# Kernel tuning notes

Measured on AMD Instinct MI355X. Metric: run time of the kernel, lower is better.

Reference implementation:

```python
import jax, jax.numpy as jnp
import numpy as np

EPS = 1e-5  # BatchNorm eps (eval mode, uses running stats)


def _conv1x1(x, W, b):
    # x: [B,C,H,W], W: [O,C], b: [O] -> [B,O,H,W]
    return jnp.einsum('bchw,oc->bohw', x, W) + b[None, :, None, None]


def setup_inputs() -> dict:
    key = jax.random.key(0)
    ks = jax.random.split(key, 13)
    B, C, M, N = 16, 512, 64, 64
    CR = C // 2
    s = 0.02
    return {
        'x': jax.random.normal(ks[0], (B, C, M, N), dtype=jnp.float32),
        'Wq': jax.random.normal(ks[1], (CR, C), dtype=jnp.float32) * s,
        'bq': jax.random.normal(ks[2], (CR,), dtype=jnp.float32) * s,
        'Wk': jax.random.normal(ks[3], (CR, C), dtype=jnp.float32) * s,
        'bk': jax.random.normal(ks[4], (CR,), dtype=jnp.float32) * s,
        'Wv': jax.random.normal(ks[5], (CR, C), dtype=jnp.float32) * s,
        'bv': jax.random.normal(ks[6], (CR,), dtype=jnp.float32) * s,
        'Wr': jax.random.normal(ks[7], (C, CR), dtype=jnp.float32) * s,
        'br': jax.random.normal(ks[8], (C,), dtype=jnp.float32) * s,
        'gamma': jax.random.normal(ks[9], (C,), dtype=jnp.float32) * 0.1 + 1.0,
        'beta': jax.random.normal(ks[10], (C,), dtype=jnp.float32) * 0.1,
        'running_mean': jax.random.normal(ks[11], (C,), dtype=jnp.float32) * 0.1,
        'running_var': jax.random.uniform(ks[12], (C,), dtype=jnp.float32, minval=0.5, maxval=1.5),
    }


def reference(x, Wq, bq, Wk, bk, Wv, bv, Wr, br, gamma, beta, running_mean, running_var):
    b, c, m, n = x.shape
    cr = Wq.shape[0]
    # 1x1-conv QKV projections
    Q = _conv1x1(x, Wq, bq).reshape(b * cr, m, n)
    K = _conv1x1(x, Wk, bk).reshape(b * cr, m, n)
    V = _conv1x1(x, Wv, bv).reshape(b * cr, m, n)
    # per-channel spatial attention over rows: [b*cr, m, m]
    corr = jnp.einsum('gik,gjk->gij', Q, K)
    attn = jax.nn.softmax(corr, axis=-1)
    y = jnp.einsum('gij,gjn->gin', attn, V).reshape(b, cr, m, n)
    # reconstruct: 1x1 conv + BatchNorm (eval mode) + residual
    y = _conv1x1(y, Wr, br)
    inv = gamma / jnp.sqrt(running_var + EPS)
    y = y * inv[None, :, None, None] + (beta - running_mean * inv)[None, :, None, None]
    return y + x
```

## Files before the change

kernel.cpp:

```cpp
#include <hip/hip_runtime.h>

typedef __attribute__((ext_vector_type(8))) short bf16x8;
typedef __attribute__((ext_vector_type(4))) float f32x4;

#define DEVI static __device__ __forceinline__

DEVI unsigned short f2b(float f) {
  union { float f; unsigned u; } v; v.f = f;
  unsigned r = v.u + 0x7fffu + ((v.u >> 16) & 1u);
  return (unsigned short)(r >> 16);
}

typedef const __attribute__((address_space(1))) void* gas1_t;
typedef __attribute__((address_space(3))) void* las3_t;
#define GL16(g, l) __builtin_amdgcn_global_load_lds((gas1_t)(g), (las3_t)(l), 16, 0, 0)

#define WAITVM(N) asm volatile("s_waitcnt vmcnt(" #N ")" ::: "memory")
#define WAITLGKM  asm volatile("s_waitcnt lgkmcnt(0)" ::: "memory")

#define OFF_WQKV  0ull
#define OFF_WR    786432ull
#define OFF_BQKV  1048576ull
#define OFF_SCALE 1051648ull
#define OFF_OFF2  1053696ull
#define OFF_XT    2097152ull
#define OFF_YT    2097152ull
#define OFF_Y     35651584ull
#define OFF_Q     69206016ull

__global__ __launch_bounds__(256) void k_prep(
    const float* __restrict__ Wq, const float* __restrict__ bq,
    const float* __restrict__ Wk, const float* __restrict__ bk,
    const float* __restrict__ Wv, const float* __restrict__ bv,
    const float* __restrict__ Wr, const float* __restrict__ br,
    const float* __restrict__ gamma, const float* __restrict__ beta,
    const float* __restrict__ rm, const float* __restrict__ rv,
    unsigned short* __restrict__ wqkv, unsigned short* __restrict__ wrb,
    float* __restrict__ bqkv, float* __restrict__ scale, float* __restrict__ off2)
{
  int i = blockIdx.x * 256 + threadIdx.x;
  if (i < 768 * 512) {
    int o = i >> 9, c = i & 511;
    float v = (o < 256) ? Wq[o * 512 + c] : (o < 512 ? Wk[(o - 256) * 512 + c] : Wv[(o - 512) * 512 + c]);
    wqkv[i] = f2b(v);
  }
  if (i < 512 * 256) wrb[i] = f2b(Wr[i]);
  if (i < 768) bqkv[i] = (i < 256) ? bq[i] : (i < 512 ? bk[i - 256] : bv[i - 512]);
  if (i < 512) {
    float inv = gamma[i] * rsqrtf(rv[i] + 1e-5f);
    scale[i] = inv;
    off2[i] = (br[i] - rm[i]) * inv + beta[i];
  }
}

__global__ __launch_bounds__(256) void k_xt(const float* __restrict__ x, unsigned short* __restrict__ xt)
{
  __shared__ unsigned short tile[64][72];
  const int b = blockIdx.z, c0 = blockIdx.y * 64, s0 = blockIdx.x * 64;
  const int t = threadIdx.x;
  const int r = t >> 2, cc = (t & 3) * 16;
  const float* src = x + ((size_t)b * 512 + c0 + r) * 4096 + s0 + cc;
  #pragma unroll
  for (int j = 0; j < 16; j += 4) {
    float4 v = *(const float4*)(src + j);
    tile[r][cc + j + 0] = f2b(v.x);
    tile[r][cc + j + 1] = f2b(v.y);
    tile[r][cc + j + 2] = f2b(v.z);
    tile[r][cc + j + 3] = f2b(v.w);
  }
  __syncthreads();
  unsigned short* dst = xt + ((size_t)b * 4096 + s0 + r) * 512 + c0 + cc;
  bf16x8 o0, o1;
  #pragma unroll
  for (int j = 0; j < 8; ++j) { o0[j] = tile[cc + j][r]; o1[j] = tile[cc + 8 + j][r]; }
  *(bf16x8*)(dst) = o0;
  *(bf16x8*)(dst + 8) = o1;
}


__global__ __launch_bounds__(256) void k_qkv(
    const unsigned short* __restrict__ xt, const unsigned short* __restrict__ wqkv,
    const float* __restrict__ bqkv, unsigned short* __restrict__ qkv)
{
  __shared__ unsigned short lds[2][2][8192];
  const int b = blockIdx.z, o0 = blockIdx.y * 128, s0 = blockIdx.x * 128;
  const int t = threadIdx.x, w = t >> 6, l = t & 63;
  const int wm = w >> 1, wn = w & 1, lr = l & 15;
  const int lkE = (l >> 4) * 8;
  const int swE = (lr & 7) * 8;
  const int cp = (t & 7) ^ ((t >> 3) & 7);

  const unsigned short* Ag = wqkv + (size_t)(o0 + (t >> 3)) * 512 + cp * 8;
  const unsigned short* Bg = xt + ((size_t)b * 4096 + s0 + (t >> 3)) * 512 + cp * 8;

  const f32x4 z = {0.f, 0.f, 0.f, 0.f};
  f32x4 acc[4][4];
  #pragma unroll
  for (int i = 0; i < 4; ++i)
    #pragma unroll
    for (int j = 0; j < 4; ++j) acc[i][j] = z;

#define STG_Q(st, kt) do { \
    _Pragma("unroll") \
    for (int j = 0; j < 4; ++j) { \
      GL16(Ag + (kt) * 64 + j * 32 * 512, (char*)&lds[st][0][0] + j * 4096 + t * 16); \
      GL16(Bg + (kt) * 64 + j * 32 * 512, (char*)&lds[st][1][0] + j * 4096 + t * 16); \
    } \
  } while (0)

#define CMP_Q(st) do { \
    const unsigned short* A  = &lds[st][0][0]; \
    const unsigned short* Bl = &lds[st][1][0]; \
    _Pragma("unroll") \
    for (int kc = 0; kc < 2; ++kc) { \
      const int kidx = (kc * 32 + lkE) ^ swE; \
      bf16x8 af[4], bfr[4]; \
      _Pragma("unroll") \
      for (int mi = 0; mi < 4; ++mi) af[mi] = *(const bf16x8*)(A + (wm * 64 + mi * 16 + lr) * 64 + kidx); \
      _Pragma("unroll") \
      for (int ni = 0; ni < 4; ++ni) bfr[ni] = *(const bf16x8*)(Bl + (wn * 64 + ni * 16 + lr) * 64 + kidx); \
      _Pragma("unroll") \
      for (int mi = 0; mi < 4; ++mi) \
        _Pragma("unroll") \
        for (int ni = 0; ni < 4; ++ni) \
          acc[mi][ni] = __builtin_amdgcn_mfma_f32_16x16x32_bf16(af[mi], bfr[ni], acc[mi][ni], 0, 0, 0); \
    } \
    WAITLGKM; __builtin_amdgcn_sched_barrier(0); \
  } while (0)

  STG_Q(0, 0); STG_Q(1, 1);
  #pragma unroll
  for (int kt = 0; kt < 7; ++kt) {
    WAITVM(8);
    __builtin_amdgcn_s_barrier();
    CMP_Q(kt & 1);
    if (kt + 2 < 8) {
      __builtin_amdgcn_s_barrier();
      STG_Q(kt & 1, kt + 2);
    }
  }
  WAITVM(0);
  __builtin_amdgcn_s_barrier();
  CMP_Q(1);

  #pragma unroll
  for (int mi = 0; mi < 4; ++mi) {
    #pragma unroll
    for (int reg = 0; reg < 4; ++reg) {
      const int o = o0 + wm * 64 + mi * 16 + (l >> 4) * 4 + reg;
      const float bias = bqkv[o];
      const size_t base = (size_t)(o >> 8) * 16777216ull + ((size_t)b * 256 + (o & 255)) * 4096;
      #pragma unroll
      for (int ni = 0; ni < 4; ++ni) {
        const int s = s0 + wn * 64 + ni * 16 + lr;
        qkv[base + s] = f2b(acc[mi][ni][reg] + bias);
      }
    }
  }
#undef STG_Q
#undef CMP_Q
}

__global__ __launch_bounds__(256) void k_attn(const unsigned short* __restrict__ qkv,
                                              unsigned short* __restrict__ yout)
{
  __shared__ unsigned short Vt[64][80];
  __shared__ unsigned short P[4][16][80];
  const int g = blockIdx.x;
  const unsigned short* qg = qkv + (size_t)g * 4096;
  const unsigned short* kg = qkv + 16777216ull + (size_t)g * 4096;
  const unsigned short* vg = qkv + 33554432ull + (size_t)g * 4096;
  const int t = threadIdx.x, w = t >> 6, l = t & 63;
  const int lr = l & 15, lk = (l >> 4) * 8;

  {
    const int j = t >> 2, c0 = (t & 3) * 16;
    bf16x8 a = *(const bf16x8*)(vg + j * 64 + c0);
    bf16x8 bb = *(const bf16x8*)(vg + j * 64 + c0 + 8);
    #pragma unroll
    for (int jj = 0; jj < 8; ++jj) { Vt[c0 + jj][j] = a[jj]; Vt[c0 + 8 + jj][j] = bb[jj]; }
  }

  const f32x4 z = {0.f, 0.f, 0.f, 0.f};
  bf16x8 qf[2];
  #pragma unroll
  for (int kc = 0; kc < 2; ++kc) qf[kc] = *(const bf16x8*)(qg + (w * 16 + lr) * 64 + kc * 32 + lk);
  f32x4 accS[4] = {z, z, z, z};
  #pragma unroll
  for (int jt = 0; jt < 4; ++jt)
    #pragma unroll
    for (int kc = 0; kc < 2; ++kc) {
      bf16x8 kf = *(const bf16x8*)(kg + (jt * 16 + lr) * 64 + kc * 32 + lk);
      accS[jt] = __builtin_amdgcn_mfma_f32_16x16x32_bf16(qf[kc], kf, accS[jt], 0, 0, 0);
    }

  #pragma unroll
  for (int reg = 0; reg < 4; ++reg) {
    float mx = fmaxf(fmaxf(accS[0][reg], accS[1][reg]), fmaxf(accS[2][reg], accS[3][reg]));
    #pragma unroll
    for (int m = 1; m < 16; m <<= 1) mx = fmaxf(mx, __shfl_xor(mx, m, 64));
    float e0 = __expf(accS[0][reg] - mx), e1 = __expf(accS[1][reg] - mx);
    float e2 = __expf(accS[2][reg] - mx), e3 = __expf(accS[3][reg] - mx);
    float sm = e0 + e1 + e2 + e3;
    #pragma unroll
    for (int m = 1; m < 16; m <<= 1) sm += __shfl_xor(sm, m, 64);
    const float rs = 1.f / sm;
    const int row = (l >> 4) * 4 + reg;
    P[w][row][0 * 16 + lr] = f2b(e0 * rs);
    P[w][row][1 * 16 + lr] = f2b(e1 * rs);
    P[w][row][2 * 16 + lr] = f2b(e2 * rs);
    P[w][row][3 * 16 + lr] = f2b(e3 * rs);
  }
  __syncthreads();

  bf16x8 pf[2];
  #pragma unroll
  for (int kc = 0; kc < 2; ++kc) pf[kc] = *(const bf16x8*)(&P[w][lr][kc * 32 + lk]);
  f32x4 accY[4] = {z, z, z, z};
  #pragma unroll
  for (int nt = 0; nt < 4; ++nt)
    #pragma unroll
    for (int kc = 0; kc < 2; ++kc) {
      bf16x8 vf = *(const bf16x8*)(&Vt[nt * 16 + lr][kc * 32 + lk]);
      accY[nt] = __builtin_amdgcn_mfma_f32_16x16x32_bf16(pf[kc], vf, accY[nt], 0, 0, 0);
    }

  unsigned short* yg = yout + (size_t)g * 4096;
  #pragma unroll
  for (int nt = 0; nt < 4; ++nt)
    #pragma unroll
    for (int reg = 0; reg < 4; ++reg) {
      const int i = w * 16 + (l >> 4) * 4 + reg;
      yg[i * 64 + nt * 16 + lr] = f2b(accY[nt][reg]);
    }
}

__global__ __launch_bounds__(256) void k_yt(const unsigned short* __restrict__ y, unsigned short* __restrict__ yt)
{
  __shared__ unsigned short tile[64][72];
  const int b = blockIdx.z, cr0 = blockIdx.y * 64, s0 = blockIdx.x * 64;
  const int t = threadIdx.x, r = t >> 2, c0 = (t & 3) * 16;
  const unsigned short* src = y + ((size_t)b * 256 + cr0 + r) * 4096 + s0 + c0;
  bf16x8 a = *(const bf16x8*)(src);
  bf16x8 bb = *(const bf16x8*)(src + 8);
  #pragma unroll
  for (int j = 0; j < 8; ++j) { tile[r][c0 + j] = a[j]; tile[r][c0 + 8 + j] = bb[j]; }
  __syncthreads();
  unsigned short* dst = yt + ((size_t)b * 4096 + s0 + r) * 256 + cr0 + c0;
  bf16x8 o0, o1;
  #pragma unroll
  for (int j = 0; j < 8; ++j) { o0[j] = tile[c0 + j][r]; o1[j] = tile[c0 + 8 + j][r]; }
  *(bf16x8*)(dst) = o0;
  *(bf16x8*)(dst + 8) = o1;
}

__global__ __launch_bounds__(256) void k_recon(
    const unsigned short* __restrict__ yt, const unsigned short* __restrict__ wrb,
    const float* __restrict__ scale, const float* __restrict__ off2,
    const float* __restrict__ x, float* __restrict__ out)
{
  __shared__ unsigned short lds[2][2][8192];
  const int b = blockIdx.z, o0 = blockIdx.y * 128, s0 = blockIdx.x * 128;
  const int t = threadIdx.x, w = t >> 6, l = t & 63;
  const int wm = w >> 1, wn = w & 1, lr = l & 15;
  const int lkE = (l >> 4) * 8;
  const int swE = (lr & 7) * 8;
  const int cp = (t & 7) ^ ((t >> 3) & 7);

  const unsigned short* Ag = wrb + (size_t)(o0 + (t >> 3)) * 256 + cp * 8;
  const unsigned short* Bg = yt + ((size_t)b * 4096 + s0 + (t >> 3)) * 256 + cp * 8;

  const f32x4 z = {0.f, 0.f, 0.f, 0.f};
  f32x4 acc[4][4];
  #pragma unroll
  for (int i = 0; i < 4; ++i)
    #pragma unroll
    for (int j = 0; j < 4; ++j) acc[i][j] = z;

#define STG_R(st, kt) do { \
    _Pragma("unroll") \
    for (int j = 0; j < 4; ++j) { \
      GL16(Ag + (kt) * 64 + j * 32 * 256, (char*)&lds[st][0][0] + j * 4096 + t * 16); \
      GL16(Bg + (kt) * 64 + j * 32 * 256, (char*)&lds[st][1][0] + j * 4096 + t * 16); \
    } \
  } while (0)

#define CMP_R(st) do { \
    const unsigned short* A  = &lds[st][0][0]; \
    const unsigned short* Bl = &lds[st][1][0]; \
    _Pragma("unroll") \
    for (int kc = 0; kc < 2; ++kc) { \
      const int kidx = (kc * 32 + lkE) ^ swE; \
      bf16x8 af[4], bfr[4]; \
      _Pragma("unroll") \
      for (int mi = 0; mi < 4; ++mi) af[mi] = *(const bf16x8*)(A + (wm * 64 + mi * 16 + lr) * 64 + kidx); \
      _Pragma("unroll") \
      for (int ni = 0; ni < 4; ++ni) bfr[ni] = *(const bf16x8*)(Bl + (wn * 64 + ni * 16 + lr) * 64 + kidx); \
      _Pragma("unroll") \
      for (int mi = 0; mi < 4; ++mi) \
        _Pragma("unroll") \
        for (int ni = 0; ni < 4; ++ni) \
          acc[mi][ni] = __builtin_amdgcn_mfma_f32_16x16x32_bf16(af[mi], bfr[ni], acc[mi][ni], 0, 0, 0); \
    } \
    WAITLGKM; __builtin_amdgcn_sched_barrier(0); \
  } while (0)

  STG_R(0, 0); STG_R(1, 1);
  #pragma unroll
  for (int kt = 0; kt < 3; ++kt) {
    WAITVM(8);
    __builtin_amdgcn_s_barrier();
    CMP_R(kt & 1);
    if (kt + 2 < 4) {
      __builtin_amdgcn_s_barrier();
      STG_R(kt & 1, kt + 2);
    }
  }
  WAITVM(0);
  __builtin_amdgcn_s_barrier();
  CMP_R(1);

  #pragma unroll
  for (int mi = 0; mi < 4; ++mi) {
    #pragma unroll
    for (int reg = 0; reg < 4; ++reg) {
      const int o = o0 + wm * 64 + mi * 16 + (l >> 4) * 4 + reg;
      const float sc = scale[o], of = off2[o];
      const size_t base = ((size_t)b * 512 + o) * 4096;
      #pragma unroll
      for (int ni = 0; ni < 4; ++ni) {
        const int s = s0 + wn * 64 + ni * 16 + lr;
        const size_t idx = base + s;
        out[idx] = acc[mi][ni][reg] * sc + of + x[idx];
      }
    }
  }
#undef STG_R
#undef CMP_R
}

extern "C" void kernel_launch(void* const* d_in, const int* in_sizes, int n_in,
                              void* d_out, int out_size, void* d_ws, size_t ws_size,
                              hipStream_t stream)
{
  const float* x     = (const float*)d_in[0];
  const float* Wq    = (const float*)d_in[1];
  const float* bq    = (const float*)d_in[2];
  const float* Wk    = (const float*)d_in[3];
  const float* bk    = (const float*)d_in[4];
  const float* Wv    = (const float*)d_in[5];
  const float* bv    = (const float*)d_in[6];
  const float* Wr    = (const float*)d_in[7];
  const float* br    = (const float*)d_in[8];
  const float* gamma = (const float*)d_in[9];
  const float* beta  = (const float*)d_in[10];
  const float* rm    = (const float*)d_in[11];
  const float* rv    = (const float*)d_in[12];

  char* ws = (char*)d_ws;
  unsigned short* wqkv  = (unsigned short*)(ws + OFF_WQKV);
  unsigned short* wrb   = (unsigned short*)(ws + OFF_WR);
  float* bqkv  = (float*)(ws + OFF_BQKV);
  float* scale = (float*)(ws + OFF_SCALE);
  float* off2  = (float*)(ws + OFF_OFF2);
  unsigned short* xt  = (unsigned short*)(ws + OFF_XT);
  unsigned short* yt  = (unsigned short*)(ws + OFF_YT);
  unsigned short* yb  = (unsigned short*)(ws + OFF_Y);
  unsigned short* qkv = (unsigned short*)(ws + OFF_Q);
  float* out = (float*)d_out;

  hipLaunchKernelGGL(k_prep, dim3(1536), dim3(256), 0, stream,
                     Wq, bq, Wk, bk, Wv, bv, Wr, br, gamma, beta, rm, rv,
                     wqkv, wrb, bqkv, scale, off2);
  hipLaunchKernelGGL(k_xt, dim3(64, 8, 16), dim3(256), 0, stream, x, xt);
  hipLaunchKernelGGL(k_qkv, dim3(32, 6, 16), dim3(256), 0, stream, xt, wqkv, bqkv, qkv);
  hipLaunchKernelGGL(k_attn, dim3(4096), dim3(256), 0, stream, qkv, yb);
  hipLaunchKernelGGL(k_yt, dim3(64, 4, 16), dim3(256), 0, stream, yb, yt);
  hipLaunchKernelGGL(k_recon, dim3(32, 4, 16), dim3(256), 0, stream, yt, wrb, scale, off2, x, out);
}
```

Before: 212.5 us.

## Fuse weight prep into transpose, drop y transpose by loading channel-major tiles in recon

Weight conversion and BN folding are merged into the x-transpose kernel, so one launch does both. The separate y transpose kernel is removed: the reconstruction GEMM now reads y in its native channel-major layout through registers into a padded LDS tile and gathers B fragments with strided scalar LDS reads. The QKV GEMM loop preloads both k-chunks' fragments before issuing MFMAs and places sched barriers around the barriers. This removes a kernel launch and a full write and read of y, in exchange for slower element-wise LDS gathers and more register pressure in recon.

```diff
diff --git a/kernel.cpp b/kernel.cpp
--- a/kernel.cpp
+++ b/kernel.cpp
@@ -17,6 +17,7 @@
 
 #define WAITVM(N) asm volatile("s_waitcnt vmcnt(" #N ")" ::: "memory")
 #define WAITLGKM  asm volatile("s_waitcnt lgkmcnt(0)" ::: "memory")
+#define SCHEDBAR  __builtin_amdgcn_sched_barrier(0)
 
 #define OFF_WQKV  0ull
 #define OFF_WR    786432ull
@@ -24,11 +25,11 @@
 #define OFF_SCALE 1051648ull
 #define OFF_OFF2  1053696ull
 #define OFF_XT    2097152ull
-#define OFF_YT    2097152ull
 #define OFF_Y     35651584ull
 #define OFF_Q     69206016ull
 
-__global__ __launch_bounds__(256) void k_prep(
+__global__ __launch_bounds__(256) void k_xt(
+    const float* __restrict__ x, unsigned short* __restrict__ xt,
     const float* __restrict__ Wq, const float* __restrict__ bq,
     const float* __restrict__ Wk, const float* __restrict__ bk,
     const float* __restrict__ Wv, const float* __restrict__ bv,
@@ -38,26 +39,27 @@
     unsigned short* __restrict__ wqkv, unsigned short* __restrict__ wrb,
     float* __restrict__ bqkv, float* __restrict__ scale, float* __restrict__ off2)
 {
-  int i = blockIdx.x * 256 + threadIdx.x;
-  if (i < 768 * 512) {
-    int o = i >> 9, c = i & 511;
-    float v = (o < 256) ? Wq[o * 512 + c] : (o < 512 ? Wk[(o - 256) * 512 + c] : Wv[(o - 512) * 512 + c]);
-    wqkv[i] = f2b(v);
-  }
-  if (i < 512 * 256) wrb[i] = f2b(Wr[i]);
-  if (i < 768) bqkv[i] = (i < 256) ? bq[i] : (i < 512 ? bk[i - 256] : bv[i - 512]);
-  if (i < 512) {
-    float inv = gamma[i] * rsqrtf(rv[i] + 1e-5f);
-    scale[i] = inv;
-    off2[i] = (br[i] - rm[i]) * inv + beta[i];
-  }
-}
-
-__global__ __launch_bounds__(256) void k_xt(const float* __restrict__ x, unsigned short* __restrict__ xt)
-{
   __shared__ unsigned short tile[64][72];
+  const int t = threadIdx.x;
+  const int bid = blockIdx.x + blockIdx.y * 64 + blockIdx.z * 512;
+
+  if (bid < 1536) {
+    int i = bid * 256 + t;
+    if (i < 768 * 512) {
+      int o = i >> 9, c = i & 511;
+      float v = (o < 256) ? Wq[o * 512 + c] : (o < 512 ? Wk[(o - 256) * 512 + c] : Wv[(o - 512) * 512 + c]);
+      wqkv[i] = f2b(v);
+    }
+    if (i < 512 * 256) wrb[i] = f2b(Wr[i]);
+    if (i < 768) bqkv[i] = (i < 256) ? bq[i] : (i < 512 ? bk[i - 256] : bv[i - 512]);
+    if (i < 512) {
+      float inv = gamma[i] * rsqrtf(rv[i] + 1e-5f);
+      scale[i] = inv;
+      off2[i] = (br[i] - rm[i]) * inv + beta[i];
+    }
+  }
+
   const int b = blockIdx.z, c0 = blockIdx.y * 64, s0 = blockIdx.x * 64;
-  const int t = threadIdx.x;
   const int r = t >> 2, cc = (t & 3) * 16;
   const float* src = x + ((size_t)b * 512 + c0 + r) * 4096 + s0 + cc;
   #pragma unroll
@@ -76,7 +78,6 @@
   *(bf16x8*)(dst) = o0;
   *(bf16x8*)(dst + 8) = o1;
 }
-
 
 __global__ __launch_bounds__(256) void k_qkv(
     const unsigned short* __restrict__ xt, const unsigned short* __restrict__ wqkv,
@@ -111,36 +112,35 @@
 #define CMP_Q(st) do { \
     const unsigned short* A  = &lds[st][0][0]; \
     const unsigned short* Bl = &lds[st][1][0]; \
+    bf16x8 af[2][4], bfr[2][4]; \
     _Pragma("unroll") \
     for (int kc = 0; kc < 2; ++kc) { \
       const int kidx = (kc * 32 + lkE) ^ swE; \
-      bf16x8 af[4], bfr[4]; \
-      _Pragma("unroll") \
-      for (int mi = 0; mi < 4; ++mi) af[mi] = *(const bf16x8*)(A + (wm * 64 + mi * 16 + lr) * 64 + kidx); \
-      _Pragma("unroll") \
-      for (int ni = 0; ni < 4; ++ni) bfr[ni] = *(const bf16x8*)(Bl + (wn * 64 + ni * 16 + lr) * 64 + kidx); \
+      _Pragma("unroll") \
+      for (int mi = 0; mi < 4; ++mi) af[kc][mi] = *(const bf16x8*)(A + (wm * 64 + mi * 16 + lr) * 64 + kidx); \
+      _Pragma("unroll") \
+      for (int ni = 0; ni < 4; ++ni) bfr[kc][ni] = *(const bf16x8*)(Bl + (wn * 64 + ni * 16 + lr) * 64 + kidx); \
+    } \
+    _Pragma("unroll") \
+    for (int kc = 0; kc < 2; ++kc) \
       _Pragma("unroll") \
       for (int mi = 0; mi < 4; ++mi) \
         _Pragma("unroll") \
         for (int ni = 0; ni < 4; ++ni) \
-          acc[mi][ni] = __builtin_amdgcn_mfma_f32_16x16x32_bf16(af[mi], bfr[ni], acc[mi][ni], 0, 0, 0); \
-    } \
-    WAITLGKM; __builtin_amdgcn_sched_barrier(0); \
+          acc[mi][ni] = __builtin_amdgcn_mfma_f32_16x16x32_bf16(af[kc][mi], bfr[kc][ni], acc[mi][ni], 0, 0, 0); \
   } while (0)
 
   STG_Q(0, 0); STG_Q(1, 1);
   #pragma unroll
   for (int kt = 0; kt < 7; ++kt) {
     WAITVM(8);
-    __builtin_amdgcn_s_barrier();
+    __builtin_amdgcn_s_barrier(); SCHEDBAR;
     CMP_Q(kt & 1);
-    if (kt + 2 < 8) {
-      __builtin_amdgcn_s_barrier();
-      STG_Q(kt & 1, kt + 2);
-    }
+    __builtin_amdgcn_s_barrier(); SCHEDBAR;
+    if (kt + 2 < 8) STG_Q(kt & 1, kt + 2);
   }
   WAITVM(0);
-  __builtin_amdgcn_s_barrier();
+  __builtin_amdgcn_s_barrier(); SCHEDBAR;
   CMP_Q(1);
 
   #pragma unroll
@@ -235,31 +235,13 @@
     }
 }
 
-__global__ __launch_bounds__(256) void k_yt(const unsigned short* __restrict__ y, unsigned short* __restrict__ yt)
-{
-  __shared__ unsigned short tile[64][72];
-  const int b = blockIdx.z, cr0 = blockIdx.y * 64, s0 = blockIdx.x * 64;
-  const int t = threadIdx.x, r = t >> 2, c0 = (t & 3) * 16;
-  const unsigned short* src = y + ((size_t)b * 256 + cr0 + r) * 4096 + s0 + c0;
-  bf16x8 a = *(const bf16x8*)(src);
-  bf16x8 bb = *(const bf16x8*)(src + 8);
-  #pragma unroll
-  for (int j = 0; j < 8; ++j) { tile[r][c0 + j] = a[j]; tile[r][c0 + 8 + j] = bb[j]; }
-  __syncthreads();
-  unsigned short* dst = yt + ((size_t)b * 4096 + s0 + r) * 256 + cr0 + c0;
-  bf16x8 o0, o1;
-  #pragma unroll
-  for (int j = 0; j < 8; ++j) { o0[j] = tile[c0 + j][r]; o1[j] = tile[c0 + 8 + j][r]; }
-  *(bf16x8*)(dst) = o0;
-  *(bf16x8*)(dst + 8) = o1;
-}
-
 __global__ __launch_bounds__(256) void k_recon(
-    const unsigned short* __restrict__ yt, const unsigned short* __restrict__ wrb,
+    const unsigned short* __restrict__ y, const unsigned short* __restrict__ wrb,
     const float* __restrict__ scale, const float* __restrict__ off2,
     const float* __restrict__ x, float* __restrict__ out)
 {
-  __shared__ unsigned short lds[2][2][8192];
+  __shared__ unsigned short Alds[2][8192];
+  __shared__ unsigned short Blds[2][64][136];
   const int b = blockIdx.z, o0 = blockIdx.y * 128, s0 = blockIdx.x * 128;
   const int t = threadIdx.x, w = t >> 6, l = t & 63;
   const int wm = w >> 1, wn = w & 1, lr = l & 15;
@@ -268,7 +250,28 @@
   const int cp = (t & 7) ^ ((t >> 3) & 7);
 
   const unsigned short* Ag = wrb + (size_t)(o0 + (t >> 3)) * 256 + cp * 8;
-  const unsigned short* Bg = yt + ((size_t)b * 4096 + s0 + (t >> 3)) * 256 + cp * 8;
+  const unsigned short* Bg = y + ((size_t)b * 256 + (t >> 2)) * 4096 + s0 + (t & 3) * 32;
+  const int brow = t >> 2, bcol = (t & 3) * 32;
+
+#define STG_A(st, kt) do { \
+    _Pragma("unroll") \
+    for (int j = 0; j < 4; ++j) \
+      GL16(Ag + (kt) * 64 + j * 32 * 256, (char*)&Alds[st][0] + j * 4096 + t * 16); \
+  } while (0)
+
+#define BLOAD(r0, r1, r2, r3, kt) do { \
+    r0 = *(const uint4*)(Bg + (size_t)(kt) * 64 * 4096 + 0); \
+    r1 = *(const uint4*)(Bg + (size_t)(kt) * 64 * 4096 + 8); \
+    r2 = *(const uint4*)(Bg + (size_t)(kt) * 64 * 4096 + 16); \
+    r3 = *(const uint4*)(Bg + (size_t)(kt) * 64 * 4096 + 24); \
+  } while (0)
+
+#define BWRITE(st, r0, r1, r2, r3) do { \
+    *(uint4*)&Blds[st][brow][bcol + 0]  = r0; \
+    *(uint4*)&Blds[st][brow][bcol + 8]  = r1; \
+    *(uint4*)&Blds[st][brow][bcol + 16] = r2; \
+    *(uint4*)&Blds[st][brow][bcol + 24] = r3; \
+  } while (0)
 
   const f32x4 z = {0.f, 0.f, 0.f, 0.f};
   f32x4 acc[4][4];
@@ -277,47 +280,58 @@
     #pragma unroll
     for (int j = 0; j < 4; ++j) acc[i][j] = z;
 
-#define STG_R(st, kt) do { \
-    _Pragma("unroll") \
-    for (int j = 0; j < 4; ++j) { \
-      GL16(Ag + (kt) * 64 + j * 32 * 256, (char*)&lds[st][0][0] + j * 4096 + t * 16); \
-      GL16(Bg + (kt) * 64 + j * 32 * 256, (char*)&lds[st][1][0] + j * 4096 + t * 16); \
-    } \
-  } while (0)
-
 #define CMP_R(st) do { \
-    const unsigned short* A  = &lds[st][0][0]; \
-    const unsigned short* Bl = &lds[st][1][0]; \
     _Pragma("unroll") \
     for (int kc = 0; kc < 2; ++kc) { \
-      const int kidx = (kc * 32 + lkE) ^ swE; \
+      const int kidxA = (kc * 32 + lkE) ^ swE; \
       bf16x8 af[4], bfr[4]; \
       _Pragma("unroll") \
-      for (int mi = 0; mi < 4; ++mi) af[mi] = *(const bf16x8*)(A + (wm * 64 + mi * 16 + lr) * 64 + kidx); \
-      _Pragma("unroll") \
-      for (int ni = 0; ni < 4; ++ni) bfr[ni] = *(const bf16x8*)(Bl + (wn * 64 + ni * 16 + lr) * 64 + kidx); \
+      for (int mi = 0; mi < 4; ++mi) af[mi] = *(const bf16x8*)(&Alds[st][0] + (wm * 64 + mi * 16 + lr) * 64 + kidxA); \
+      _Pragma("unroll") \
+      for (int ni = 0; ni < 4; ++ni) { \
+        const int scol = wn * 64 + ni * 16 + lr; \
+        _Pragma("unroll") \
+        for (int e = 0; e < 8; ++e) bfr[ni][e] = (short)Blds[st][kc * 32 + lkE + e][scol]; \
+      } \
       _Pragma("unroll") \
       for (int mi = 0; mi < 4; ++mi) \
         _Pragma("unroll") \
         for (int ni = 0; ni < 4; ++ni) \
           acc[mi][ni] = __builtin_amdgcn_mfma_f32_16x16x32_bf16(af[mi], bfr[ni], acc[mi][ni], 0, 0, 0); \
     } \
-    WAITLGKM; __builtin_amdgcn_sched_barrier(0); \
-  } while (0)
-
-  STG_R(0, 0); STG_R(1, 1);
-  #pragma unroll
-  for (int kt = 0; kt < 3; ++kt) {
-    WAITVM(8);
-    __builtin_amdgcn_s_barrier();
-    CMP_R(kt & 1);
-    if (kt + 2 < 4) {
-      __builtin_amdgcn_s_barrier();
-      STG_R(kt & 1, kt + 2);
-    }
-  }
+  } while (0)
+
+  uint4 a0, a1, a2, a3, b0, b1, b2, b3;
+  STG_A(0, 0);           SCHEDBAR;
+  BLOAD(a0, a1, a2, a3, 0); SCHEDBAR;
+  STG_A(1, 1);           SCHEDBAR;
+  BLOAD(b0, b1, b2, b3, 1); SCHEDBAR;
+  WAITVM(8);
+  BWRITE(0, a0, a1, a2, a3);
+  WAITLGKM;
+  __builtin_amdgcn_s_barrier(); SCHEDBAR;
+  CMP_R(0);
+  __builtin_amdgcn_s_barrier(); SCHEDBAR;
+  STG_A(0, 2); SCHEDBAR;
+  BLOAD(a0, a1, a2, a3, 2); SCHEDBAR;
+  WAITVM(8);
+  BWRITE(1, b0, b1, b2, b3);
+  WAITLGKM;
+  __builtin_amdgcn_s_barrier(); SCHEDBAR;
+  CMP_R(1);
+  __builtin_amdgcn_s_barrier(); SCHEDBAR;
+  STG_A(1, 3); SCHEDBAR;
+  BLOAD(b0, b1, b2, b3, 3); SCHEDBAR;
+  WAITVM(8);
+  BWRITE(0, a0, a1, a2, a3);
+  WAITLGKM;
+  __builtin_amdgcn_s_barrier(); SCHEDBAR;
+  CMP_R(0);
+  __builtin_amdgcn_s_barrier(); SCHEDBAR;
   WAITVM(0);
-  __builtin_amdgcn_s_barrier();
+  BWRITE(1, b0, b1, b2, b3);
+  WAITLGKM;
+  __builtin_amdgcn_s_barrier(); SCHEDBAR;
   CMP_R(1);
 
   #pragma unroll
@@ -335,7 +349,9 @@
       }
     }
   }
-#undef STG_R
+#undef STG_A
+#undef BLOAD
+#undef BWRITE
 #undef CMP_R
 }
 
@@ -364,17 +380,14 @@
   float* scale = (float*)(ws + OFF_SCALE);
   float* off2  = (float*)(ws + OFF_OFF2);
   unsigned short* xt  = (unsigned short*)(ws + OFF_XT);
-  unsigned short* yt  = (unsigned short*)(ws + OFF_YT);
   unsigned short* yb  = (unsigned short*)(ws + OFF_Y);
   unsigned short* qkv = (unsigned short*)(ws + OFF_Q);
   float* out = (float*)d_out;
 
-  hipLaunchKernelGGL(k_prep, dim3(1536), dim3(256), 0, stream,
-                     Wq, bq, Wk, bk, Wv, bv, Wr, br, gamma, beta, rm, rv,
+  hipLaunchKernelGGL(k_xt, dim3(64, 8, 16), dim3(256), 0, stream,
+                     x, xt, Wq, bq, Wk, bk, Wv, bv, Wr, br, gamma, beta, rm, rv,
                      wqkv, wrb, bqkv, scale, off2);
-  hipLaunchKernelGGL(k_xt, dim3(64, 8, 16), dim3(256), 0, stream, x, xt);
   hipLaunchKernelGGL(k_qkv, dim3(32, 6, 16), dim3(256), 0, stream, xt, wqkv, bqkv, qkv);
   hipLaunchKernelGGL(k_attn, dim3(4096), dim3(256), 0, stream, qkv, yb);
-  hipLaunchKernelGGL(k_yt, dim3(64, 4, 16), dim3(256), 0, stream, yb, yt);
-  hipLaunchKernelGGL(k_recon, dim3(32, 4, 16), dim3(256), 0, stream, yt, wrb, scale, off2, x, out);
-}
+  hipLaunchKernelGGL(k_recon, dim3(32, 4, 16), dim3(256), 0, stream, yb, wrb, scale, off2, x, out);
+}
```

Measured after the change: 201.7 us. 5.1% less time.
